# Kernel optimization log

Hardware: AMD Instinct MI355X
Metric: run time of the kernel (lower is better)

The kernel has to match this reference:

```python
import jax, jax.numpy as jnp
import numpy as np

B, N, K, H, C = 16, 2048, 9, 128, 2  # K = nb_neighbors, kernel_size = K+1


def setup_inputs() -> dict:
    key = jax.random.key(0)
    ks = jax.random.split(key, 7)
    s = 0.1
    x = jax.random.normal(ks[0], (B, N, C), jnp.float32)
    Wconv = jax.random.normal(ks[1], (H, C, K + 1), jnp.float32) * s  # conv1d weight
    bconv = jax.random.normal(ks[2], (H,), jnp.float32) * s
    W1 = jax.random.normal(ks[3], (H, C), jnp.float32) * s
    b1 = jax.random.normal(ks[4], (H,), jnp.float32) * s
    W2 = jax.random.normal(ks[5], (H, H), jnp.float32) * s
    b2 = jax.random.normal(ks[6], (H,), jnp.float32) * s
    return {"x": x, "Wconv": Wconv, "bconv": bconv, "W1": W1, "b1": b1, "W2": W2, "b2": b2}


def reference(x, Wconv, bconv, W1, b1, W2, b2):
    # node embedding: W1(x)
    node_emb = jnp.einsum('bnc,hc->bnh', x, W1) + b1  # (B,N,H)

    # pairwise Euclidean distances (B,N,N) via the GEMM form
    sq = jnp.sum(x * x, axis=-1)  # (B,N)
    d2 = sq[:, :, None] + sq[:, None, :] - 2.0 * jnp.einsum('bnc,bmc->bnm', x, x)
    dist = jnp.sqrt(jnp.maximum(d2, 0.0))

    # torch: topk(k=N) (descending) then take last K+1 columns -> the K+1
    # smallest distances ordered descending (nearest/self last)
    knn = jnp.flip(jnp.argsort(dist, axis=-1)[..., : K + 1], axis=-1)  # (B,N,K+1)

    # batched gather of neighbor coords: (B,N,K+1,C)
    coords = jax.vmap(lambda xb, ib: xb[ib])(x, knn)

    # conv1d with kernel spanning the full window -> single output position,
    # i.e. a contraction over (channel, position)
    conv_emb = jnp.einsum('bnkc,hck->bnh', coords, Wconv) + bconv  # (B,N,H)
    conv_emb = jnp.einsum('bnh,eh->bne', conv_emb, W2) + b2

    return node_emb + conv_emb
```

## Files before the change

kernel.cpp:

```cpp
#include <hip/hip_runtime.h>
#include <cfloat>
#include <stdint.h>

#define B_   16
#define N_   2048
#define KK   10
#define H_   128
#define SUB  32
#define NCH  (N_ / SUB)

#define RANK_BLOCKS (B_ * 32)
#define WEFF_OUT    (H_ * KK * 2 + H_)
#define WEFF_BLOCKS ((WEFF_OUT * 4) / 256)

__device__ inline uint32_t f32_ordered(float f) {
    uint32_t u = __float_as_uint(f);
    return (u & 0x80000000u) ? ~u : (u | 0x80000000u);
}

__global__ __launch_bounds__(256) void setup_kernel(
    const float* __restrict__ x,
    const float* __restrict__ Wconv, const float* __restrict__ bconv,
    const float* __restrict__ b1,    const float* __restrict__ W2,
    const float* __restrict__ b2,
    float4* __restrict__ xsorted,
    float*  __restrict__ weff,
    float*  __restrict__ btot)
{
#pragma clang fp contract(off)
    __shared__ __align__(16) uint64_t sk[N_];
    __shared__ int pcnt[4 * 64];
    const int tid = threadIdx.x;

    if (blockIdx.x >= RANK_BLOCKS) {
        const int g = (blockIdx.x - RANK_BLOCKS) * 256 + tid;
        const int o = g >> 2, q = g & 3;
        float acc = 0.f;
        if (o < H_ * KK * 2) {
            const int e = o / 20, r = o % 20, k = r >> 1, c = r & 1;
            const float* w2p = W2 + e * H_ + q * 32;
            const float* wcp = Wconv + (q * 32) * (2 * KK) + c * KK + k;
#pragma unroll 8
            for (int h = 0; h < 32; ++h)
                acc += w2p[h] * wcp[h * (2 * KK)];
        } else {
            const int e = o - H_ * KK * 2;
            const float* w2p = W2 + e * H_ + q * 32;
            const float* bcp = bconv + q * 32;
#pragma unroll 8
            for (int h = 0; h < 32; ++h) acc += w2p[h] * bcp[h];
        }
        acc += __shfl_xor(acc, 1, 64);
        acc += __shfl_xor(acc, 2, 64);
        if (q == 0) {
            if (o < H_ * KK * 2) weff[o] = acc;
            else {
                const int e = o - H_ * KK * 2;
                btot[e] = acc + b1[e] + b2[e];
            }
        }
        return;
    }

    const int b  = blockIdx.x >> 5;
    const int sg = blockIdx.x & 31;
    const float2* xb = (const float2*)(x + (size_t)b * N_ * 2);

    for (int i = tid; i < N_; i += 256)
        sk[i] = ((uint64_t)f32_ordered(xb[i].x) << 32) | (uint32_t)i;
    __syncthreads();

    const int el = tid & 63;
    const int pt = tid >> 6;
    const uint64_t kown = sk[sg * 64 + el];
    const ulonglong2* sk2 = (const ulonglong2*)sk + pt * 256;
    int cnt = 0;
#pragma unroll 2
    for (int j = 0; j < 256; j += 4) {
        ulonglong2 t0 = sk2[j + 0];
        ulonglong2 t1 = sk2[j + 1];
        ulonglong2 t2 = sk2[j + 2];
        ulonglong2 t3 = sk2[j + 3];
        cnt += (int)(t0.x < kown) + (int)(t0.y < kown)
             + (int)(t1.x < kown) + (int)(t1.y < kown)
             + (int)(t2.x < kown) + (int)(t2.y < kown)
             + (int)(t3.x < kown) + (int)(t3.y < kown);
    }
    pcnt[pt * 64 + el] = cnt;
    __syncthreads();

    if (tid < 64) {
        const int r = pcnt[tid] + pcnt[64 + tid] + pcnt[128 + tid] + pcnt[192 + tid];
        const int i = sg * 64 + tid;
        float2 p = xb[i];
        float sm = p.x * p.x + p.y * p.y;
        xsorted[(size_t)b * N_ + r] =
            make_float4(p.x, p.y, sm, __uint_as_float((uint32_t)i));
    }
}

__global__ __launch_bounds__(512, 4) void knn_conv_kernel(
    const float4* __restrict__ xsorted,
    const float* __restrict__ W1,
    const float* __restrict__ weff,
    const float* __restrict__ btot,
    float* __restrict__ out)
{
#pragma clang fp contract(off)
    __shared__ float4   xs4[N_];
    __shared__ uint64_t mkeys[64 * 81];
    __shared__ float    wcoord[64 * 21];
    __shared__ float    hbound[8 * 64];

    const int tid  = threadIdx.x;
    const int w    = tid >> 6;
    const int l    = tid & 63;
    const int b    = blockIdx.x >> 5;
    const int tile = blockIdx.x & 31;

    const float4* xb = xsorted + (size_t)b * N_;
    for (int i = tid; i < N_; i += 512) xs4[i] = xb[i];
    __syncthreads();

    const int    n  = tile * 64 + l;
    const float4 qv = xs4[n];
    const float  qx = qv.x, qy = qv.y, sqn = qv.z;
    const float  qa  = xs4[tile * 64].x;
    const float  qbx = xs4[tile * 64 + 63].x;

    const uint64_t KINIT = (((uint64_t)0x7F7FFFFFu) << 32) | 0x3FFFFFu;
    uint64_t hk[KK];
#pragma unroll
    for (int j = 0; j < KK; ++j) hk[j] = KINIT;
    float h9d  = FLT_MAX;
    float shb  = FLT_MAX;
    float gate = FLT_MAX;

    auto insert = [&](float dc, float cw, int m) {
        uint32_t oi = __float_as_uint(cw);
        uint64_t key = ((uint64_t)__float_as_uint(dc) << 32)
                     | (oi << 11) | (uint32_t)m;
        if (key < hk[KK - 1]) {
#pragma unroll
            for (int j = KK - 1; j >= 1; --j) {
                bool cj  = key < hk[j];
                bool cjm = key < hk[j - 1];
                hk[j] = cj ? (cjm ? hk[j - 1] : key) : hk[j];
            }
            hk[0] = (key < hk[0]) ? key : hk[0];
        }
        h9d  = __uint_as_float((uint32_t)(hk[KK - 1] >> 32));
        gate = fminf(h9d, shb);
    };

    auto scan_chunk = [&](int mc) {
        for (int mm = 0; mm < SUB; mm += 4) {
            const int m0 = mc + mm;
            float4 c0 = xs4[m0 + 0];
            float4 c1 = xs4[m0 + 1];
            float4 c2 = xs4[m0 + 2];
            float4 c3 = xs4[m0 + 3];
            float dc0, dc1, dc2, dc3;
            { float s = sqn + c0.z; float pr = qx * c0.x;
              float dt = __builtin_fmaf(qy, c0.y, pr);
              float d2 = __builtin_fmaf(-2.0f, dt, s); dc0 = d2 > 0.0f ? d2 : 0.0f; }
            { float s = sqn + c1.z; float pr = qx * c1.x;
              float dt = __builtin_fmaf(qy, c1.y, pr);
              float d2 = __builtin_fmaf(-2.0f, dt, s); dc1 = d2 > 0.0f ? d2 : 0.0f; }
            { float s = sqn + c2.z; float pr = qx * c2.x;
              float dt = __builtin_fmaf(qy, c2.y, pr);
              float d2 = __builtin_fmaf(-2.0f, dt, s); dc2 = d2 > 0.0f ? d2 : 0.0f; }
            { float s = sqn + c3.z; float pr = qx * c3.x;
              float dt = __builtin_fmaf(qy, c3.y, pr);
              float d2 = __builtin_fmaf(-2.0f, dt, s); dc3 = d2 > 0.0f ? d2 : 0.0f; }
            if (dc0 <= gate) insert(dc0, c0.w, m0 + 0);
            if (dc1 <= gate) insert(dc1, c1.w, m0 + 1);
            if (dc2 <= gate) insert(dc2, c2.w, m0 + 2);
            if (dc3 <= gate) insert(dc3, c3.w, m0 + 3);
        }
    };

    const int ct2 = 2 * tile;
    const int a   = (w - ct2) & 7;
    const int c1_ = ct2 + a;
    const int c2_ = c1_ - 8;
    int c_near = (a <= 4) ? c1_ : c2_;
    if (c1_ > NCH - 1) c_near = c2_;
    if (c2_ < 0)       c_near = c1_;
    scan_chunk(c_near * SUB);

    hbound[w * 64 + l] = h9d;
    __syncthreads();
    {
        float m0 = fminf(hbound[0 * 64 + l], hbound[1 * 64 + l]);
        float m1 = fminf(hbound[2 * 64 + l], hbound[3 * 64 + l]);
        float m2 = fminf(hbound[4 * 64 + l], hbound[5 * 64 + l]);
        float m3 = fminf(hbound[6 * 64 + l], hbound[7 * 64 + l]);
        shb  = fminf(fminf(m0, m1), fminf(m2, m3));
        gate = fminf(h9d, shb);
    }

    int  cl = c_near - 8, cr = c_near + 8;
    bool la = (cl >= 0), ra = (cr <= NCH - 1);
    while (la || ra) {
        float wm = gate;
        wm = fmaxf(wm, __shfl_xor(wm, 1,  64));
        wm = fmaxf(wm, __shfl_xor(wm, 2,  64));
        wm = fmaxf(wm, __shfl_xor(wm, 4,  64));
        wm = fmaxf(wm, __shfl_xor(wm, 8,  64));
        wm = fmaxf(wm, __shfl_xor(wm, 16, 64));
        wm = fmaxf(wm, __shfl_xor(wm, 32, 64));
        float gl = la ? (qa - xs4[cl * SUB + SUB - 1].x) : FLT_MAX;
        float gr = ra ? (xs4[cr * SUB].x - qbx)          : FLT_MAX;
        bool pickL = la && (!ra || gl <= gr);
        if (pickL) {
            if (__builtin_fmaf(gl, gl, -4e-6f) > wm) la = false;
            else { scan_chunk(cl * SUB); cl -= 8; la = (cl >= 0); }
        } else {
            if (__builtin_fmaf(gr, gr, -4e-6f) > wm) ra = false;
            else { scan_chunk(cr * SUB); cr += 8; ra = (cr <= NCH - 1); }
        }
    }

    {
        const int mb = l * 81 + w * 10;
#pragma unroll
        for (int j = 0; j < KK; ++j) mkeys[mb + j] = hk[j];
    }

    const int e = tid & 127;
    float we[20];
    {
        const float4* wp = (const float4*)(weff + e * 20);
#pragma unroll
        for (int r = 0; r < 5; ++r) {
            float4 v = wp[r];
            we[4 * r + 0] = v.x; we[4 * r + 1] = v.y;
            we[4 * r + 2] = v.z; we[4 * r + 3] = v.w;
        }
    }
    const float w1x = W1[e * 2 + 0];
    const float w1y = W1[e * 2 + 1];
    const float bt  = btot[e];
    __syncthreads();

    {
        const int q = tid >> 3;
        const int r = tid & 7;
        const int mb = q * 81 + r * 10;
        int p = 0;
#pragma unroll
        for (int sel = 0; sel < KK; ++sel) {
            uint64_t v = (p < KK) ? mkeys[mb + p] : 0xFFFFFFFFFFFFFFFFull;
            uint64_t t1 = __shfl_xor((unsigned long long)v, 1, 64);
            uint64_t m1 = v  < t1 ? v  : t1;
            uint64_t t2 = __shfl_xor((unsigned long long)m1, 2, 64);
            uint64_t m2 = m1 < t2 ? m1 : t2;
            uint64_t t4 = __shfl_xor((unsigned long long)m2, 4, 64);
            uint64_t vm = m2 < t4 ? m2 : t4;
            if (v == vm) {
                ++p;
                float4 c = xs4[(int)(vm & 0x7FF)];
                const int k = (KK - 1) - sel;
                wcoord[q * 21 + 2 * k + 0] = c.x;
                wcoord[q * 21 + 2 * k + 1] = c.y;
            }
        }
    }
    __syncthreads();

    const int qb_ = tid >> 7;
    const size_t obase = (size_t)b * N_ * H_;
#pragma unroll
    for (int jj = 0; jj < 16; ++jj) {
        const int qq = qb_ + 4 * jj;
        float4 xq = xs4[tile * 64 + qq];
        uint32_t orig = __float_as_uint(xq.w);
        const float* wc = &wcoord[qq * 21];
        float acc = bt;
        acc += xq.x * w1x;
        acc += xq.y * w1y;
#pragma unroll
        for (int k = 0; k < KK; ++k) {
            acc += wc[2 * k + 0] * we[2 * k + 0];
            acc += wc[2 * k + 1] * we[2 * k + 1];
        }
        out[obase + (size_t)orig * H_ + e] = acc;
    }
}

extern "C" void kernel_launch(void* const* d_in, const int* in_sizes, int n_in,
                              void* d_out, int out_size, void* d_ws, size_t ws_size,
                              hipStream_t stream) {
    const float* x     = (const float*)d_in[0];
    const float* Wconv = (const float*)d_in[1];
    const float* bconv = (const float*)d_in[2];
    const float* W1    = (const float*)d_in[3];
    const float* b1    = (const float*)d_in[4];
    const float* W2    = (const float*)d_in[5];
    const float* b2    = (const float*)d_in[6];
    float* out  = (float*)d_out;
    float* weff = (float*)d_ws;
    float* btot = weff + H_ * KK * 2;
    float4* xsorted = (float4*)((char*)d_ws + 16384);

    setup_kernel<<<dim3(RANK_BLOCKS + WEFF_BLOCKS), dim3(256), 0, stream>>>(
        x, Wconv, bconv, b1, W2, b2, xsorted, weff, btot);
    knn_conv_kernel<<<dim3(B_ * (N_ / 64)), dim3(512), 0, stream>>>(
        xsorted, W1, weff, btot, out);
}
```

Baseline: 143.0 us.

## Halve query tile per block and split each chunk scan across two half-wavefronts

The kNN kernel now uses 256-thread blocks, each handling 32 queries instead of 64, so the grid doubles. Each query's candidate search is still divided eight ways: four wavefronts times two half-wavefronts, each half scanning interleaved columns of a 32-point chunk, with the chunk stride changed from 8 to 4. The smaller query tile spans a narrower x-range, which should let the distance-bound pruning stop scanning earlier, and it spreads the work over more blocks. In exchange, every block still copies the whole 2048-point batch into LDS, so total shared-memory fill traffic doubles.

Measured after the change: 169.0 us. 18.1% more time.

```diff
diff --git a/kernel.cpp b/kernel.cpp
--- a/kernel.cpp
+++ b/kernel.cpp
@@ -99,7 +99,7 @@
     }
 }
 
-__global__ __launch_bounds__(512, 4) void knn_conv_kernel(
+__global__ __launch_bounds__(256, 2) void knn_conv_kernel(
     const float4* __restrict__ xsorted,
     const float* __restrict__ W1,
     const float* __restrict__ weff,
@@ -108,25 +108,27 @@
 {
 #pragma clang fp contract(off)
     __shared__ float4   xs4[N_];
-    __shared__ uint64_t mkeys[64 * 81];
-    __shared__ float    wcoord[64 * 21];
-    __shared__ float    hbound[8 * 64];
+    __shared__ uint64_t mkeys[32 * 81];
+    __shared__ float    wcoord[32 * 21];
+    __shared__ float    hbound[32 * 9];
 
     const int tid  = threadIdx.x;
     const int w    = tid >> 6;
     const int l    = tid & 63;
-    const int b    = blockIdx.x >> 5;
-    const int tile = blockIdx.x & 31;
+    const int q    = l & 31;
+    const int hh   = l >> 5;
+    const int b    = blockIdx.x >> 6;
+    const int tile = blockIdx.x & 63;
 
     const float4* xb = xsorted + (size_t)b * N_;
-    for (int i = tid; i < N_; i += 512) xs4[i] = xb[i];
-    __syncthreads();
-
-    const int    n  = tile * 64 + l;
+    for (int i = tid; i < N_; i += 256) xs4[i] = xb[i];
+    __syncthreads();
+
+    const int    n  = tile * 32 + q;
     const float4 qv = xs4[n];
     const float  qx = qv.x, qy = qv.y, sqn = qv.z;
-    const float  qa  = xs4[tile * 64].x;
-    const float  qbx = xs4[tile * 64 + 63].x;
+    const float  qa  = xs4[tile * 32].x;
+    const float  qbx = xs4[tile * 32 + 31].x;
 
     const uint64_t KINIT = (((uint64_t)0x7F7FFFFFu) << 32) | 0x3FFFFFu;
     uint64_t hk[KK];
@@ -154,12 +156,14 @@
     };
 
     auto scan_chunk = [&](int mc) {
-        for (int mm = 0; mm < SUB; mm += 4) {
-            const int m0 = mc + mm;
+        const int base = mc + hh;
+#pragma unroll
+        for (int jj = 0; jj < 4; ++jj) {
+            const int m0 = base + jj * 8;
             float4 c0 = xs4[m0 + 0];
-            float4 c1 = xs4[m0 + 1];
-            float4 c2 = xs4[m0 + 2];
-            float4 c3 = xs4[m0 + 3];
+            float4 c1 = xs4[m0 + 2];
+            float4 c2 = xs4[m0 + 4];
+            float4 c3 = xs4[m0 + 6];
             float dc0, dc1, dc2, dc3;
             { float s = sqn + c0.z; float pr = qx * c0.x;
               float dt = __builtin_fmaf(qy, c0.y, pr);
@@ -174,33 +178,34 @@
               float dt = __builtin_fmaf(qy, c3.y, pr);
               float d2 = __builtin_fmaf(-2.0f, dt, s); dc3 = d2 > 0.0f ? d2 : 0.0f; }
             if (dc0 <= gate) insert(dc0, c0.w, m0 + 0);
-            if (dc1 <= gate) insert(dc1, c1.w, m0 + 1);
-            if (dc2 <= gate) insert(dc2, c2.w, m0 + 2);
-            if (dc3 <= gate) insert(dc3, c3.w, m0 + 3);
+            if (dc1 <= gate) insert(dc1, c1.w, m0 + 2);
+            if (dc2 <= gate) insert(dc2, c2.w, m0 + 4);
+            if (dc3 <= gate) insert(dc3, c3.w, m0 + 6);
         }
     };
 
-    const int ct2 = 2 * tile;
-    const int a   = (w - ct2) & 7;
-    const int c1_ = ct2 + a;
-    const int c2_ = c1_ - 8;
-    int c_near = (a <= 4) ? c1_ : c2_;
+    const int ct  = tile;
+    const int a   = (w - ct) & 3;
+    const int c1_ = ct + a;
+    const int c2_ = c1_ - 4;
+    int c_near = (a <= 2) ? c1_ : c2_;
     if (c1_ > NCH - 1) c_near = c2_;
     if (c2_ < 0)       c_near = c1_;
     scan_chunk(c_near * SUB);
 
-    hbound[w * 64 + l] = h9d;
+    hbound[q * 9 + (w * 2 + hh)] = h9d;
     __syncthreads();
     {
-        float m0 = fminf(hbound[0 * 64 + l], hbound[1 * 64 + l]);
-        float m1 = fminf(hbound[2 * 64 + l], hbound[3 * 64 + l]);
-        float m2 = fminf(hbound[4 * 64 + l], hbound[5 * 64 + l]);
-        float m3 = fminf(hbound[6 * 64 + l], hbound[7 * 64 + l]);
+        const float* hb = &hbound[q * 9];
+        float m0 = fminf(hb[0], hb[1]);
+        float m1 = fminf(hb[2], hb[3]);
+        float m2 = fminf(hb[4], hb[5]);
+        float m3 = fminf(hb[6], hb[7]);
         shb  = fminf(fminf(m0, m1), fminf(m2, m3));
         gate = fminf(h9d, shb);
     }
 
-    int  cl = c_near - 8, cr = c_near + 8;
+    int  cl = c_near - 4, cr = c_near + 4;
     bool la = (cl >= 0), ra = (cr <= NCH - 1);
     while (la || ra) {
         float wm = gate;
@@ -215,15 +220,15 @@
         bool pickL = la && (!ra || gl <= gr);
         if (pickL) {
             if (__builtin_fmaf(gl, gl, -4e-6f) > wm) la = false;
-            else { scan_chunk(cl * SUB); cl -= 8; la = (cl >= 0); }
+            else { scan_chunk(cl * SUB); cl -= 4; la = (cl >= 0); }
         } else {
             if (__builtin_fmaf(gr, gr, -4e-6f) > wm) ra = false;
-            else { scan_chunk(cr * SUB); cr += 8; ra = (cr <= NCH - 1); }
+            else { scan_chunk(cr * SUB); cr += 4; ra = (cr <= NCH - 1); }
         }
     }
 
     {
-        const int mb = l * 81 + w * 10;
+        const int mb = q * 81 + (w * 2 + hh) * 10;
 #pragma unroll
         for (int j = 0; j < KK; ++j) mkeys[mb + j] = hk[j];
     }
@@ -245,9 +250,9 @@
     __syncthreads();
 
     {
-        const int q = tid >> 3;
-        const int r = tid & 7;
-        const int mb = q * 81 + r * 10;
+        const int qm = tid >> 3;
+        const int r  = tid & 7;
+        const int mb = qm * 81 + r * 10;
         int p = 0;
 #pragma unroll
         for (int sel = 0; sel < KK; ++sel) {
@@ -262,8 +267,8 @@
                 ++p;
                 float4 c = xs4[(int)(vm & 0x7FF)];
                 const int k = (KK - 1) - sel;
-                wcoord[q * 21 + 2 * k + 0] = c.x;
-                wcoord[q * 21 + 2 * k + 1] = c.y;
+                wcoord[qm * 21 + 2 * k + 0] = c.x;
+                wcoord[qm * 21 + 2 * k + 1] = c.y;
             }
         }
     }
@@ -273,8 +278,8 @@
     const size_t obase = (size_t)b * N_ * H_;
 #pragma unroll
     for (int jj = 0; jj < 16; ++jj) {
-        const int qq = qb_ + 4 * jj;
-        float4 xq = xs4[tile * 64 + qq];
+        const int qq = qb_ + 2 * jj;
+        float4 xq = xs4[tile * 32 + qq];
         uint32_t orig = __float_as_uint(xq.w);
         const float* wc = &wcoord[qq * 21];
         float acc = bt;
@@ -306,6 +311,6 @@
 
     setup_kernel<<<dim3(RANK_BLOCKS + WEFF_BLOCKS), dim3(256), 0, stream>>>(
         x, Wconv, bconv, b1, W2, b2, xsorted, weff, btot);
-    knn_conv_kernel<<<dim3(B_ * (N_ / 64)), dim3(512), 0, stream>>>(
+    knn_conv_kernel<<<dim3(B_ * NCH), dim3(256), 0, stream>>>(
         xsorted, W1, weff, btot, out);
 }
```

## Split each query across 8 lanes scanning interleaved candidates, merge via shuffles

Applied to the files above, without the earlier changes.

Restructures the kNN search so each query is owned by an 8-lane group within one wavefront, with each lane scanning a strided quarter of every 32-point chunk. The search runs outward from the query's home chunks one chunk at a time instead of striding across warps. The shared-memory bound exchange, the key staging buffer and a block barrier are replaced by intra-group shuffles, and merging now pops directly from register heaps. This cuts LDS traffic and synchronisation and tightens pruning per query, but adds shuffle overhead on every loop iteration and pruning now uses the bounds of 8-query groups.

Result: slower. 150.9 us (+5.5%).

```diff
diff --git a/kernel.cpp b/kernel.cpp
--- a/kernel.cpp
+++ b/kernel.cpp
@@ -107,14 +107,13 @@
     float* __restrict__ out)
 {
 #pragma clang fp contract(off)
-    __shared__ float4   xs4[N_];
-    __shared__ uint64_t mkeys[64 * 81];
-    __shared__ float    wcoord[64 * 21];
-    __shared__ float    hbound[8 * 64];
+    __shared__ float4 xs4[N_];
+    __shared__ float  wcoord[64 * 21];
 
     const int tid  = threadIdx.x;
     const int w    = tid >> 6;
-    const int l    = tid & 63;
+    const int r    = tid & 7;
+    const int qm   = tid >> 3;
     const int b    = blockIdx.x >> 5;
     const int tile = blockIdx.x & 31;
 
@@ -122,11 +121,11 @@
     for (int i = tid; i < N_; i += 512) xs4[i] = xb[i];
     __syncthreads();
 
-    const int    n  = tile * 64 + l;
-    const float4 qv = xs4[n];
+    const float4 qv = xs4[tile * 64 + qm];
     const float  qx = qv.x, qy = qv.y, sqn = qv.z;
-    const float  qa  = xs4[tile * 64].x;
-    const float  qbx = xs4[tile * 64 + 63].x;
+    const int    gfirst = tile * 64 + w * 8;
+    const float  qa  = xs4[gfirst].x;
+    const float  qbx = xs4[gfirst + 7].x;
 
     const uint64_t KINIT = (((uint64_t)0x7F7FFFFFu) << 32) | 0x3FFFFFu;
     uint64_t hk[KK];
@@ -154,78 +153,65 @@
     };
 
     auto scan_chunk = [&](int mc) {
-        for (int mm = 0; mm < SUB; mm += 4) {
-            const int m0 = mc + mm;
-            float4 c0 = xs4[m0 + 0];
-            float4 c1 = xs4[m0 + 1];
-            float4 c2 = xs4[m0 + 2];
-            float4 c3 = xs4[m0 + 3];
-            float dc0, dc1, dc2, dc3;
-            { float s = sqn + c0.z; float pr = qx * c0.x;
-              float dt = __builtin_fmaf(qy, c0.y, pr);
-              float d2 = __builtin_fmaf(-2.0f, dt, s); dc0 = d2 > 0.0f ? d2 : 0.0f; }
-            { float s = sqn + c1.z; float pr = qx * c1.x;
-              float dt = __builtin_fmaf(qy, c1.y, pr);
-              float d2 = __builtin_fmaf(-2.0f, dt, s); dc1 = d2 > 0.0f ? d2 : 0.0f; }
-            { float s = sqn + c2.z; float pr = qx * c2.x;
-              float dt = __builtin_fmaf(qy, c2.y, pr);
-              float d2 = __builtin_fmaf(-2.0f, dt, s); dc2 = d2 > 0.0f ? d2 : 0.0f; }
-            { float s = sqn + c3.z; float pr = qx * c3.x;
-              float dt = __builtin_fmaf(qy, c3.y, pr);
-              float d2 = __builtin_fmaf(-2.0f, dt, s); dc3 = d2 > 0.0f ? d2 : 0.0f; }
-            if (dc0 <= gate) insert(dc0, c0.w, m0 + 0);
-            if (dc1 <= gate) insert(dc1, c1.w, m0 + 1);
-            if (dc2 <= gate) insert(dc2, c2.w, m0 + 2);
-            if (dc3 <= gate) insert(dc3, c3.w, m0 + 3);
-        }
+        const int m0 = mc + r;
+        float4 c0 = xs4[m0 + 0];
+        float4 c1 = xs4[m0 + 8];
+        float4 c2 = xs4[m0 + 16];
+        float4 c3 = xs4[m0 + 24];
+        float dc0, dc1, dc2, dc3;
+        { float s = sqn + c0.z; float pr = qx * c0.x;
+          float dt = __builtin_fmaf(qy, c0.y, pr);
+          float d2 = __builtin_fmaf(-2.0f, dt, s); dc0 = d2 > 0.0f ? d2 : 0.0f; }
+        { float s = sqn + c1.z; float pr = qx * c1.x;
+          float dt = __builtin_fmaf(qy, c1.y, pr);
+          float d2 = __builtin_fmaf(-2.0f, dt, s); dc1 = d2 > 0.0f ? d2 : 0.0f; }
+        { float s = sqn + c2.z; float pr = qx * c2.x;
+          float dt = __builtin_fmaf(qy, c2.y, pr);
+          float d2 = __builtin_fmaf(-2.0f, dt, s); dc2 = d2 > 0.0f ? d2 : 0.0f; }
+        { float s = sqn + c3.z; float pr = qx * c3.x;
+          float dt = __builtin_fmaf(qy, c3.y, pr);
+          float d2 = __builtin_fmaf(-2.0f, dt, s); dc3 = d2 > 0.0f ? d2 : 0.0f; }
+        if (dc0 <= gate) insert(dc0, c0.w, m0 + 0);
+        if (dc1 <= gate) insert(dc1, c1.w, m0 + 8);
+        if (dc2 <= gate) insert(dc2, c2.w, m0 + 16);
+        if (dc3 <= gate) insert(dc3, c3.w, m0 + 24);
     };
 
-    const int ct2 = 2 * tile;
-    const int a   = (w - ct2) & 7;
-    const int c1_ = ct2 + a;
-    const int c2_ = c1_ - 8;
-    int c_near = (a <= 4) ? c1_ : c2_;
-    if (c1_ > NCH - 1) c_near = c2_;
-    if (c2_ < 0)       c_near = c1_;
-    scan_chunk(c_near * SUB);
-
-    hbound[w * 64 + l] = h9d;
-    __syncthreads();
-    {
-        float m0 = fminf(hbound[0 * 64 + l], hbound[1 * 64 + l]);
-        float m1 = fminf(hbound[2 * 64 + l], hbound[3 * 64 + l]);
-        float m2 = fminf(hbound[4 * 64 + l], hbound[5 * 64 + l]);
-        float m3 = fminf(hbound[6 * 64 + l], hbound[7 * 64 + l]);
-        shb  = fminf(fminf(m0, m1), fminf(m2, m3));
-        gate = fminf(h9d, shb);
-    }
-
-    int  cl = c_near - 8, cr = c_near + 8;
-    bool la = (cl >= 0), ra = (cr <= NCH - 1);
-    while (la || ra) {
-        float wm = gate;
-        wm = fmaxf(wm, __shfl_xor(wm, 1,  64));
-        wm = fmaxf(wm, __shfl_xor(wm, 2,  64));
-        wm = fmaxf(wm, __shfl_xor(wm, 4,  64));
+    auto bounds = [&]() {
+        float gb = h9d;
+        gb = fminf(gb, __shfl_xor(gb, 1, 64));
+        gb = fminf(gb, __shfl_xor(gb, 2, 64));
+        gb = fminf(gb, __shfl_xor(gb, 4, 64));
+        shb = gb; gate = fminf(h9d, gb);
+        float wm = gb;
         wm = fmaxf(wm, __shfl_xor(wm, 8,  64));
         wm = fmaxf(wm, __shfl_xor(wm, 16, 64));
         wm = fmaxf(wm, __shfl_xor(wm, 32, 64));
-        float gl = la ? (qa - xs4[cl * SUB + SUB - 1].x) : FLT_MAX;
-        float gr = ra ? (xs4[cr * SUB].x - qbx)          : FLT_MAX;
-        bool pickL = la && (!ra || gl <= gr);
-        if (pickL) {
+        return wm;
+    };
+
+    const int home = tile * 2 + (w >> 2);
+    int c0s = home - 1;
+    if (c0s < 0) c0s = 0;
+    if (c0s > NCH - 3) c0s = NCH - 3;
+    scan_chunk((c0s + 0) * SUB);
+    scan_chunk((c0s + 1) * SUB);
+    scan_chunk((c0s + 2) * SUB);
+
+    int  cl = c0s - 1, cr = c0s + 3;
+    bool la = (cl >= 0), ra = (cr <= NCH - 1);
+    while (la || ra) {
+        float wm = bounds();
+        if (la) {
+            float gl = qa - xs4[cl * SUB + SUB - 1].x;
             if (__builtin_fmaf(gl, gl, -4e-6f) > wm) la = false;
-            else { scan_chunk(cl * SUB); cl -= 8; la = (cl >= 0); }
-        } else {
+            else { scan_chunk(cl * SUB); cl -= 1; la = (cl >= 0); }
+        }
+        if (ra) {
+            float gr = xs4[cr * SUB].x - qbx;
             if (__builtin_fmaf(gr, gr, -4e-6f) > wm) ra = false;
-            else { scan_chunk(cr * SUB); cr += 8; ra = (cr <= NCH - 1); }
-        }
-    }
-
-    {
-        const int mb = l * 81 + w * 10;
-#pragma unroll
-        for (int j = 0; j < KK; ++j) mkeys[mb + j] = hk[j];
+            else { scan_chunk(cr * SUB); cr += 1; ra = (cr <= NCH - 1); }
+        }
     }
 
     const int e = tid & 127;
@@ -233,25 +219,20 @@
     {
         const float4* wp = (const float4*)(weff + e * 20);
 #pragma unroll
-        for (int r = 0; r < 5; ++r) {
-            float4 v = wp[r];
-            we[4 * r + 0] = v.x; we[4 * r + 1] = v.y;
-            we[4 * r + 2] = v.z; we[4 * r + 3] = v.w;
+        for (int rr = 0; rr < 5; ++rr) {
+            float4 v = wp[rr];
+            we[4 * rr + 0] = v.x; we[4 * rr + 1] = v.y;
+            we[4 * rr + 2] = v.z; we[4 * rr + 3] = v.w;
         }
     }
     const float w1x = W1[e * 2 + 0];
     const float w1y = W1[e * 2 + 1];
     const float bt  = btot[e];
-    __syncthreads();
 
     {
-        const int q = tid >> 3;
-        const int r = tid & 7;
-        const int mb = q * 81 + r * 10;
-        int p = 0;
 #pragma unroll
         for (int sel = 0; sel < KK; ++sel) {
-            uint64_t v = (p < KK) ? mkeys[mb + p] : 0xFFFFFFFFFFFFFFFFull;
+            uint64_t v  = hk[0];
             uint64_t t1 = __shfl_xor((unsigned long long)v, 1, 64);
             uint64_t m1 = v  < t1 ? v  : t1;
             uint64_t t2 = __shfl_xor((unsigned long long)m1, 2, 64);
@@ -259,11 +240,13 @@
             uint64_t t4 = __shfl_xor((unsigned long long)m2, 4, 64);
             uint64_t vm = m2 < t4 ? m2 : t4;
             if (v == vm) {
-                ++p;
+#pragma unroll
+                for (int j = 0; j < KK - 1; ++j) hk[j] = hk[j + 1];
+                hk[KK - 1] = 0xFFFFFFFFFFFFFFFFull;
                 float4 c = xs4[(int)(vm & 0x7FF)];
                 const int k = (KK - 1) - sel;
-                wcoord[q * 21 + 2 * k + 0] = c.x;
-                wcoord[q * 21 + 2 * k + 1] = c.y;
+                wcoord[qm * 21 + 2 * k + 0] = c.x;
+                wcoord[qm * 21 + 2 * k + 1] = c.y;
             }
         }
     }
```
